# Kernel optimization log

Measured on AMD Instinct MI355X. Metric: run time of the kernel, lower is better.

## Reference

```python
import jax, jax.numpy as jnp
import numpy as np

B, S, D, H = 2, 2048, 1024, 16
DK = D // H

def setup_inputs() -> dict:
    key = jax.random.key(0)
    ks = jax.random.split(key, 11)
    s = 1.0 / np.sqrt(D)
    inp = {
        'q': jax.random.normal(ks[0], (B, S, D), jnp.float32),
        'k': jax.random.normal(ks[1], (B, S, D), jnp.float32),
        'v': jax.random.normal(ks[2], (B, S, D), jnp.float32),
        'mask': jnp.tril(jnp.ones((S, S), jnp.bool_))[None, None],  # [1,1,S,S] causal
        'w_q': jax.random.normal(ks[3], (D, D), jnp.float32) * s,
        'b_q': jax.random.normal(ks[4], (D,), jnp.float32) * s,
        'w_k': jax.random.normal(ks[5], (D, D), jnp.float32) * s,
        'b_k': jax.random.normal(ks[6], (D,), jnp.float32) * s,
        'w_v': jax.random.normal(ks[7], (D, D), jnp.float32) * s,
        'b_v': jax.random.normal(ks[8], (D,), jnp.float32) * s,
        'w_o': jax.random.normal(ks[9], (D, D), jnp.float32) * s,
        'b_o': jax.random.normal(ks[10], (D,), jnp.float32) * s,
    }
    return inp

def reference(q, k, v, mask, w_q, b_q, w_k, b_k, w_v, b_v, w_o, b_o):
    # Linear projections (torch Linear: x @ W^T + b)
    qh = (q @ w_q.T + b_q).reshape(B, S, H, DK).transpose(0, 2, 1, 3)  # [B,H,S,DK]
    kh = (k @ w_k.T + b_k).reshape(B, S, H, DK).transpose(0, 2, 1, 3)
    vh = (v @ w_v.T + b_v).reshape(B, S, H, DK).transpose(0, 2, 1, 3)
    scores = jnp.einsum('bhqd,bhkd->bhqk', qh, kh) / jnp.sqrt(jnp.float32(DK))
    scores = jnp.where(mask, scores, jnp.float32(-jnp.inf))
    attn = jax.nn.softmax(scores, axis=-1)  # dropout p=0.0 -> identity
    out = jnp.einsum('bhqk,bhkd->bhqd', attn, vh)
    out = out.transpose(0, 2, 1, 3).reshape(B, S, D)
    return out @ w_o.T + b_o
```

## Files before the change

### kernel.cpp

```cpp
#include <hip/hip_runtime.h>
#include <hip/hip_bf16.h>

typedef __bf16 bf16_t;
typedef __bf16 bf16x4 __attribute__((ext_vector_type(4)));
typedef __bf16 bf16x8 __attribute__((ext_vector_type(8)));
typedef float f32x4 __attribute__((ext_vector_type(4)));

#define B_ 2
#define S_ 2048
#define D_ 1024
#define H_ 16
#define DK_ 64
#define M_ (B_ * S_)

__device__ __forceinline__ f32x4 mfma16(bf16x8 a, bf16x8 b, f32x4 c) {
  return __builtin_amdgcn_mfma_f32_16x16x32_bf16(a, b, c, 0, 0, 0);
}

__device__ __forceinline__ void async_load16(const bf16_t* g, bf16_t* l) {
  __builtin_amdgcn_global_load_lds(
      (const __attribute__((address_space(1))) void*)g,
      (__attribute__((address_space(3))) void*)l, 16, 0, 0);
}


__global__ void cvt_all(const float* __restrict__ q, const float* __restrict__ k,
                        const float* __restrict__ v, const float* __restrict__ w0,
                        const float* __restrict__ w1, const float* __restrict__ w2,
                        const float* __restrict__ w3, bf16_t* __restrict__ qb,
                        bf16_t* __restrict__ kb, bf16_t* __restrict__ vb,
                        bf16_t* __restrict__ o0, bf16_t* __restrict__ o1,
                        bf16_t* __restrict__ o2, bf16_t* __restrict__ o3) {
  const int y = blockIdx.y;
  if (y >= 3 && blockIdx.x >= 512) return;
  const float* src;
  bf16_t* dst;
  float sc = 1.0f;
  switch (y) {
    case 0: src = q; dst = qb; break;
    case 1: src = k; dst = kb; break;
    case 2: src = v; dst = vb; break;
    case 3: src = w0; dst = o0; sc = 0.125f; break;
    case 4: src = w1; dst = o1; break;
    case 5: src = w2; dst = o2; break;
    default: src = w3; dst = o3; break;
  }
  long i = ((long)blockIdx.x * blockDim.x + threadIdx.x) * 8;
  const float4* s4 = (const float4*)(src + i);
  float4 a = s4[0], b = s4[1];
  bf16x8 o;
  o[0] = (bf16_t)(a.x * sc); o[1] = (bf16_t)(a.y * sc);
  o[2] = (bf16_t)(a.z * sc); o[3] = (bf16_t)(a.w * sc);
  o[4] = (bf16_t)(b.x * sc); o[5] = (bf16_t)(b.y * sc);
  o[6] = (bf16_t)(b.z * sc); o[7] = (bf16_t)(b.w * sc);
  *(bf16x8*)(dst + i) = o;
}


__device__ __forceinline__ int swzG(int b) {
  return b ^ (((b >> 7) & 7) << 4);
}

template <int NR>
__device__ __forceinline__ void stage_tile(const bf16_t* g, bf16_t* lds,
                                           const int* srcoff, int wave) {
#pragma unroll
  for (int rnd = 0; rnd < NR; ++rnd)
    async_load16(g + srcoff[rnd], lds + rnd * 2048 + wave * 512);
}

template <int MODE>
__device__ __forceinline__ void gemm_core(const bf16_t* __restrict__ A,
                                          const bf16_t* __restrict__ W,
                                          const float* __restrict__ bias,
                                          float bscale, void* __restrict__ Cv,
                                          bf16_t* __restrict__ As,
                                          bf16_t* __restrict__ Bs) {
  constexpr int N = 1024, K = 1024;
  constexpr int TILE = 128 * 32;
  constexpr int NIT = K / 32;
  const int tid = threadIdx.x;
  const int wave = tid >> 6, lane = tid & 63;
  const int quad = lane >> 4, l15 = lane & 15;
  const int wm = wave >> 1, wn = wave & 1;
  const int bm = blockIdx.x * 128, bn = blockIdx.y * 128;

  f32x4 acc[4][4] = {};

  int srcoff[2];
#pragma unroll
  for (int rnd = 0; rnd < 2; ++rnd) {
    const int bb = rnd * 4096 + tid * 16;
    const int sb = swzG(bb);
    srcoff[rnd] = (sb >> 6) * K + ((sb & 63) >> 1);
  }
  const bf16_t* ag = A + (long)bm * K;
  const bf16_t* bg = W + (long)bn * K;

  const int xorv = ((l15 >> 1) & 7) << 4;
  const int aco = (((wm * 64 + l15) * 64 + quad * 16) ^ xorv) >> 1;
  const int bco = (((wn * 64 + l15) * 64 + quad * 16) ^ xorv) >> 1;

  stage_tile<2>(ag, As, srcoff, wave);
  stage_tile<2>(bg, Bs, srcoff, wave);
  stage_tile<2>(ag + 32, As + TILE, srcoff, wave);
  stage_tile<2>(bg + 32, Bs + TILE, srcoff, wave);

  int rb = 0, sb2 = 2;
  for (int j = 0; j < NIT; ++j) {
    if (j < NIT - 1)
      asm volatile("s_waitcnt vmcnt(4)" ::: "memory");
    else
      asm volatile("s_waitcnt vmcnt(0)" ::: "memory");
    __builtin_amdgcn_sched_barrier(0);
    __builtin_amdgcn_s_barrier();
    __builtin_amdgcn_sched_barrier(0);

    if (j + 2 < NIT) {
      const int kk2 = (j + 2) * 32;
      stage_tile<2>(ag + kk2, As + sb2 * TILE, srcoff, wave);
      stage_tile<2>(bg + kk2, Bs + sb2 * TILE, srcoff, wave);
    }
    sb2 = (sb2 == 2) ? 0 : sb2 + 1;

    const bf16_t* Ac = As + rb * TILE;
    const bf16_t* Bc = Bs + rb * TILE;
    rb = (rb == 2) ? 0 : rb + 1;
    bf16x8 af[4], bfr[4];
#pragma unroll
    for (int i = 0; i < 4; ++i)
      af[i] = *(const bf16x8*)&Ac[aco + i * 512];
#pragma unroll
    for (int i = 0; i < 4; ++i)
      bfr[i] = *(const bf16x8*)&Bc[bco + i * 512];
    __builtin_amdgcn_s_setprio(1);
#pragma unroll
    for (int mi = 0; mi < 4; ++mi)
#pragma unroll
      for (int ni = 0; ni < 4; ++ni)
        acc[mi][ni] = mfma16(af[mi], bfr[ni], acc[mi][ni]);
    __builtin_amdgcn_s_setprio(0);
  }

#pragma unroll
  for (int mi = 0; mi < 4; ++mi) {
#pragma unroll
    for (int ni = 0; ni < 4; ++ni) {
      const int col = bn + wn * 64 + ni * 16 + l15;
      const float bsv = bias[col] * bscale;
      f32x4 v = acc[mi][ni];
      const int row0 = bm + wm * 64 + mi * 16 + quad * 4;
      if (MODE == 3) {
        float* C = (float*)Cv;
#pragma unroll
        for (int r = 0; r < 4; ++r)
          C[(long)(row0 + r) * N + col] = v[r] + bsv;
      } else if (MODE == 1) {
        bf16_t* C = (bf16_t*)Cv;
        const int hh = col >> 6, dk = col & 63;
        const int bq = row0 >> 11, s0 = row0 & 2047;
        bf16_t* base = C + (((long)bq * H_ + hh) * S_ + s0) * DK_ + dk;
#pragma unroll
        for (int r = 0; r < 4; ++r)
          base[(long)r * DK_] = (bf16_t)(v[r] + bsv);
      } else {
        bf16_t* C = (bf16_t*)Cv;
        const int hh = col >> 6, dk = col & 63;
        const int bq = row0 >> 11, s0 = row0 & 2047;
        bf16x4 pk;
#pragma unroll
        for (int r = 0; r < 4; ++r) pk[r] = (bf16_t)(v[r] + bsv);
        *(bf16x4*)(C + (((long)bq * H_ + hh) * DK_ + dk) * S_ + s0) = pk;
      }
    }
  }
}

__global__ __launch_bounds__(256) void gemm_qkv(
    const bf16_t* __restrict__ qb, const bf16_t* __restrict__ kb,
    const bf16_t* __restrict__ vb, const bf16_t* __restrict__ wq,
    const bf16_t* __restrict__ wk, const bf16_t* __restrict__ wv,
    const float* __restrict__ biq, const float* __restrict__ bik,
    const float* __restrict__ biv, bf16_t* __restrict__ Qh,
    bf16_t* __restrict__ Kh, bf16_t* __restrict__ Vt) {
  __shared__ bf16_t As[3][128 * 32];
  __shared__ bf16_t Bs[3][128 * 32];
  if (blockIdx.z == 0)
    gemm_core<1>(qb, wq, biq, 0.125f, Qh, &As[0][0], &Bs[0][0]);
  else if (blockIdx.z == 1)
    gemm_core<1>(kb, wk, bik, 1.0f, Kh, &As[0][0], &Bs[0][0]);
  else
    gemm_core<2>(vb, wv, biv, 1.0f, Vt, &As[0][0], &Bs[0][0]);
}

__device__ __forceinline__ int swzG128(int b) {
  return b ^ (((b >> 7) & 7) << 4);
}

__global__ __launch_bounds__(256) void gemm_out64(
    const bf16_t* __restrict__ AO, const bf16_t* __restrict__ wo,
    const float* __restrict__ bo, float* __restrict__ out) {
  constexpr int N = 1024, K = 1024;
  constexpr int ATILE = 64 * 64, BTILE = 128 * 64;
  constexpr int NIT = K / 64;
  __shared__ bf16_t As[3][ATILE];
  __shared__ bf16_t Bs[3][BTILE];
  const int tid = threadIdx.x;
  const int wave = tid >> 6, lane = tid & 63;
  const int quad = lane >> 4, l15 = lane & 15;
  const int wm = wave >> 1, wn = wave & 1;
  const int bm = blockIdx.x * 64, bn = blockIdx.y * 128;

  f32x4 acc[2][4] = {};

  int srcoff[4];
#pragma unroll
  for (int rnd = 0; rnd < 4; ++rnd) {
    const int bb = rnd * 4096 + tid * 16;
    const int sb = swzG128(bb);
    srcoff[rnd] = (sb >> 7) * K + ((sb & 127) >> 1);
  }
  const bf16_t* ag = AO + (long)bm * K;
  const bf16_t* bg = wo + (long)bn * K;

  const int co0 = ((quad * 16) ^ ((l15 & 7) << 4)) >> 1;
  const int co1 = ((quad * 16 + 64) ^ ((l15 & 7) << 4)) >> 1;
  const int arow0 = (wm * 32 + l15) * 64;
  const int brow0 = (wn * 64 + l15) * 64;

  stage_tile<2>(ag, &As[0][0], srcoff, wave);
  stage_tile<4>(bg, &Bs[0][0], srcoff, wave);
  stage_tile<2>(ag + 64, &As[1][0], srcoff, wave);
  stage_tile<4>(bg + 64, &Bs[1][0], srcoff, wave);

  int rb = 0, sb2 = 2;
  for (int j = 0; j < NIT; ++j) {
    if (j < NIT - 1)
      asm volatile("s_waitcnt vmcnt(6)" ::: "memory");
    else
      asm volatile("s_waitcnt vmcnt(0)" ::: "memory");
    __builtin_amdgcn_sched_barrier(0);
    __builtin_amdgcn_s_barrier();
    __builtin_amdgcn_sched_barrier(0);

    if (j + 2 < NIT) {
      const int kk2 = (j + 2) * 64;
      stage_tile<2>(ag + kk2, &As[sb2][0], srcoff, wave);
      stage_tile<4>(bg + kk2, &Bs[sb2][0], srcoff, wave);
    }
    sb2 = (sb2 == 2) ? 0 : sb2 + 1;

    const bf16_t* Ac = &As[rb][0];
    const bf16_t* Bc = &Bs[rb][0];
    rb = (rb == 2) ? 0 : rb + 1;
#pragma unroll
    for (int h = 0; h < 2; ++h) {
      const int co = h ? co1 : co0;
      bf16x8 af[2], bfr[4];
#pragma unroll
      for (int i = 0; i < 2; ++i)
        af[i] = *(const bf16x8*)&Ac[arow0 + i * 1024 + co];
#pragma unroll
      for (int i = 0; i < 4; ++i)
        bfr[i] = *(const bf16x8*)&Bc[brow0 + i * 1024 + co];
      __builtin_amdgcn_s_setprio(1);
#pragma unroll
      for (int mi = 0; mi < 2; ++mi)
#pragma unroll
        for (int ni = 0; ni < 4; ++ni)
          acc[mi][ni] = mfma16(af[mi], bfr[ni], acc[mi][ni]);
      __builtin_amdgcn_s_setprio(0);
    }
  }

#pragma unroll
  for (int mi = 0; mi < 2; ++mi) {
#pragma unroll
    for (int ni = 0; ni < 4; ++ni) {
      const int col = bn + wn * 64 + ni * 16 + l15;
      const float bsv = bo[col];
      f32x4 v = acc[mi][ni];
      const int row0 = bm + wm * 32 + mi * 16 + quad * 4;
#pragma unroll
      for (int r = 0; r < 4; ++r)
        out[(long)(row0 + r) * N + col] = v[r] + bsv;
    }
  }
}


__device__ __forceinline__ int swzK(int b) {
  return b ^ (((b >> 7) & 3) << 4) ^ (((b >> 10) & 1) << 6);
}
__device__ __forceinline__ int swzV(int b) {
  return b ^ (((b >> 7) & 7) << 4);
}

template <bool MASKED>
__device__ __forceinline__ void softmax_pa(const f32x4 st[4], float& l_i,
                                           bf16x8& pa0, bf16x8& pa1,
                                           const int qcol, const int quad) {
#pragma unroll
  for (int nb = 0; nb < 4; ++nb) {
    const int kvb = quad * 8 + (nb & 1) * 4 + (nb >> 1) * 32;
#pragma unroll
    for (int r = 0; r < 4; ++r) {
      float x = st[nb][r];
      if (MASKED && (kvb + r) > qcol) x = -30000.f;
      const float pv = __expf(x);
      l_i += pv;
      const bf16_t pb = (bf16_t)pv;
      const int idx = ((nb & 1) << 2) | r;
      if (nb < 2) pa0[idx] = pb;
      else        pa1[idx] = pb;
    }
  }
}

__global__ __launch_bounds__(256, 3) void flash_attn3(
    const bf16_t* __restrict__ Qh, const bf16_t* __restrict__ Kh,
    const bf16_t* __restrict__ Vt, bf16_t* __restrict__ Po,
    float* __restrict__ Pl) {
  const int bid = blockIdx.x;
  const int g = bid & 31;
  const int z = bid >> 5;
  const int i = z / 3, pi = z % 3;
  const int h = g & 15, b = g >> 4;
  const int tA = i, tB = 31 - i;
  const int tid = threadIdx.x, wave = tid >> 6, lane = tid & 63;
  const int quad = lane >> 4, l15 = lane & 15;
  const int qcol = wave * 16 + l15;
  const int prow = ((l15 >> 2) << 3) | (l15 & 3);

  __shared__ bf16_t Kls[2][64 * 64];
  __shared__ bf16_t Vls[2][64 * 64];

  const bf16_t* qhead = Qh + ((long)(b * H_ + h) * S_) * DK_;
  const bf16_t* khead = Kh + ((long)(b * H_ + h) * S_) * DK_;
  const bf16_t* vhead = Vt + ((long)(b * H_ + h) * DK_) * S_;

  int koffe[2], voffe[2], ldse[2];
#pragma unroll
  for (int c = 0; c < 2; ++c) {
    const int bb = c * 4096 + wave * 1024 + lane * 16;
    koffe[c] = swzK(bb) >> 1;
    const int vs = swzV(bb);
    voffe[c] = (vs >> 7) * S_ + ((vs & 127) >> 1);
    ldse[c] = c * 2048 + wave * 512;
  }

  int kro[4][2], vro[4][2];
#pragma unroll
  for (int nb = 0; nb < 4; ++nb) {
    const int krow = prow + (nb & 1) * 4 + (nb >> 1) * 32;
    const int vrow = nb * 16 + l15;
#pragma unroll
    for (int hh = 0; hh < 2; ++hh) {
      kro[nb][hh] = swzK(krow * 128 + quad * 16 + hh * 64) >> 1;
      vro[nb][hh] = swzV(vrow * 128 + quad * 16 + hh * 64) >> 1;
    }
  }

  const int qA = tA * 64 + wave * 16;
  const int qB = tB * 64 + wave * 16;
  const bf16_t* qpA = qhead + (long)(qA + l15) * DK_ + quad * 8;
  const bf16_t* qpB = qhead + (long)(qB + l15) * DK_ + quad * 8;
  const bf16x8 aqA0 = *(const bf16x8*)qpA;
  const bf16x8 aqA1 = *(const bf16x8*)(qpA + 32);
  const bf16x8 aqB0 = *(const bf16x8*)qpB;
  const bf16x8 aqB1 = *(const bf16x8*)(qpB + 32);

  f32x4 oA[4] = {}, oB[4] = {};
  float lA = 0.f, lB = 0.f;

  {
    const bf16_t* kt = khead + pi * (64 * DK_);
    const bf16_t* vt = vhead + pi * 64;
#pragma unroll
    for (int c = 0; c < 2; ++c) {
      async_load16(kt + koffe[c], &Kls[0][ldse[c]]);
      async_load16(vt + voffe[c], &Vls[0][ldse[c]]);
    }
  }

  int cur = 0;
  for (int j = pi; j <= tB; j += 3) {
    const bool pf = (j + 3 <= tB);
    if (pf) {
      const bf16_t* kt = khead + (j + 3) * (64 * DK_);
      const bf16_t* vt = vhead + (j + 3) * 64;
#pragma unroll
      for (int c = 0; c < 2; ++c) {
        async_load16(kt + koffe[c], &Kls[cur ^ 1][ldse[c]]);
        async_load16(vt + voffe[c], &Vls[cur ^ 1][ldse[c]]);
      }
      asm volatile("s_waitcnt vmcnt(4)" ::: "memory");
    } else {
      asm volatile("s_waitcnt vmcnt(0)" ::: "memory");
    }
    __builtin_amdgcn_sched_barrier(0);
    __builtin_amdgcn_s_barrier();
    __builtin_amdgcn_sched_barrier(0);

    const bf16_t* Kc = &Kls[cur][0];
    const bf16_t* Vc = &Vls[cur][0];

    bf16x8 k0[4], k1[4];
#pragma unroll
    for (int nb = 0; nb < 4; ++nb) {
      k0[nb] = *(const bf16x8*)&Kc[kro[nb][0]];
      k1[nb] = *(const bf16x8*)&Kc[kro[nb][1]];
    }

    bf16x8 paB0, paB1, paA0, paA1;
    {
      f32x4 stB[4];
#pragma unroll
      for (int nb = 0; nb < 4; ++nb) {
        f32x4 t = {};
        t = mfma16(k0[nb], aqB0, t);
        t = mfma16(k1[nb], aqB1, t);
        stB[nb] = t;
      }
      if (j == tB)
        softmax_pa<true>(stB, lB, paB0, paB1, qcol, quad);
      else
        softmax_pa<false>(stB, lB, paB0, paB1, qcol, quad);
    }
    const bool doA = (j <= tA);
    if (doA) {
      f32x4 stA[4];
#pragma unroll
      for (int nb = 0; nb < 4; ++nb) {
        f32x4 t = {};
        t = mfma16(k0[nb], aqA0, t);
        t = mfma16(k1[nb], aqA1, t);
        stA[nb] = t;
      }
      if (j == tA)
        softmax_pa<true>(stA, lA, paA0, paA1, qcol, quad);
      else
        softmax_pa<false>(stA, lA, paA0, paA1, qcol, quad);
    }

    bf16x8 v0[4], v1[4];
#pragma unroll
    for (int nb = 0; nb < 4; ++nb) {
      v0[nb] = *(const bf16x8*)&Vc[vro[nb][0]];
      v1[nb] = *(const bf16x8*)&Vc[vro[nb][1]];
    }
#pragma unroll
    for (int nb = 0; nb < 4; ++nb) {
      oB[nb] = mfma16(paB0, v0[nb], oB[nb]);
      oB[nb] = mfma16(paB1, v1[nb], oB[nb]);
    }
    if (doA) {
#pragma unroll
      for (int nb = 0; nb < 4; ++nb) {
        oA[nb] = mfma16(paA0, v0[nb], oA[nb]);
        oA[nb] = mfma16(paA1, v1[nb], oA[nb]);
      }
    }

    asm volatile("s_waitcnt lgkmcnt(0)" ::: "memory");
    __builtin_amdgcn_sched_barrier(0);
    __builtin_amdgcn_s_barrier();
    __builtin_amdgcn_sched_barrier(0);
    cur ^= 1;
  }

  lA += __shfl_xor(lA, 16, 64);
  lA += __shfl_xor(lA, 32, 64);
  lB += __shfl_xor(lB, 16, 64);
  lB += __shfl_xor(lB, 32, 64);

  bf16_t* po = Po + (long)pi * (M_ * D_);
  bf16_t* poA = po + (long)(b * S_ + qA + quad * 4) * D_ + h * DK_ + l15;
  bf16_t* poB = po + (long)(b * S_ + qB + quad * 4) * D_ + h * DK_ + l15;
#pragma unroll
  for (int r = 0; r < 4; ++r) {
#pragma unroll
    for (int nb = 0; nb < 4; ++nb) {
      poA[(long)r * D_ + nb * 16] = (bf16_t)oA[nb][r];
      poB[(long)r * D_ + nb * 16] = (bf16_t)oB[nb][r];
    }
  }

  if (quad == 0) {
    float* pl = Pl + (long)pi * (B_ * H_ * S_) + (long)(b * H_ + h) * S_;
    pl[qA + l15] = lA;
    pl[qB + l15] = lB;
  }
}


__global__ __launch_bounds__(256) void merge_po(const bf16_t* __restrict__ Po,
                                                const float* __restrict__ Pl,
                                                bf16_t* __restrict__ AO) {
  const long e = ((long)blockIdx.x * 256 + threadIdx.x) * 8;
  const int bs = (int)(e >> 10);
  const int d = (int)(e & 1023);
  const int h = d >> 6;
  const int b = bs >> 11, s = bs & 2047;
  const long lidx = ((long)(b * H_ + h)) * S_ + s;

  float acc[8] = {0.f, 0.f, 0.f, 0.f, 0.f, 0.f, 0.f, 0.f};
  float L = 0.f;
#pragma unroll
  for (int p = 0; p < 3; ++p) {
    bf16x8 x = *(const bf16x8*)(Po + (long)p * (M_ * D_) + e);
#pragma unroll
    for (int k = 0; k < 8; ++k) acc[k] += (float)x[k];
    L += Pl[(long)p * (B_ * H_ * S_) + lidx];
  }
  const float inv = 1.f / L;
  bf16x8 y;
#pragma unroll
  for (int k = 0; k < 8; ++k) y[k] = (bf16_t)(acc[k] * inv);
  *(bf16x8*)(AO + e) = y;
}


extern "C" void kernel_launch(void* const* d_in, const int* in_sizes, int n_in,
                              void* d_out, int out_size, void* d_ws, size_t ws_size,
                              hipStream_t stream) {
  const float* q = (const float*)d_in[0];
  const float* k = (const float*)d_in[1];
  const float* v = (const float*)d_in[2];
  const float* wq = (const float*)d_in[4];
  const float* bq = (const float*)d_in[5];
  const float* wk = (const float*)d_in[6];
  const float* bk = (const float*)d_in[7];
  const float* wv = (const float*)d_in[8];
  const float* bv = (const float*)d_in[9];
  const float* wo = (const float*)d_in[10];
  const float* bo = (const float*)d_in[11];
  float* out = (float*)d_out;

  char* ws = (char*)d_ws;
  const size_t MB = 1024 * 1024;
  bf16_t* Qh = (bf16_t*)(ws);
  bf16_t* Kh = (bf16_t*)(ws + 8 * MB);
  bf16_t* Vt = (bf16_t*)(ws + 16 * MB);
  bf16_t* AO = (bf16_t*)(ws + 24 * MB);
  bf16_t* qb = (bf16_t*)(ws + 32 * MB);
  bf16_t* kb = (bf16_t*)(ws + 40 * MB);
  bf16_t* vb = (bf16_t*)(ws + 48 * MB);
  bf16_t* wqb = (bf16_t*)(ws + 56 * MB);
  bf16_t* wkb = (bf16_t*)(ws + 58 * MB);
  bf16_t* wvb = (bf16_t*)(ws + 60 * MB);
  bf16_t* wob = (bf16_t*)(ws + 62 * MB);
  bf16_t* Po = (bf16_t*)(ws + 32 * MB);
  float* Pl = (float*)(ws + 56 * MB);

  cvt_all<<<dim3(2048, 7, 1), 256, 0, stream>>>(q, k, v, wq, wk, wv, wo, qb, kb,
                                                vb, wqb, wkb, wvb, wob);
  gemm_qkv<<<dim3(32, 8, 3), 256, 0, stream>>>(qb, kb, vb, wqb, wkb, wvb, bq, bk,
                                               bv, Qh, Kh, Vt);
  flash_attn3<<<dim3(1536, 1, 1), 256, 0, stream>>>(Qh, Kh, Vt, Po, Pl);
  merge_po<<<dim3(2048, 1, 1), 256, 0, stream>>>(Po, Pl, AO);
  gemm_out64<<<dim3(64, 8, 1), 256, 0, stream>>>(AO, wob, bo, out);
}
```

Before: 216.9 us.

## Fuse partial-output merge into output GEMM and triple-buffer flash attention K/V

Removes the merge_po kernel. The output-projection GEMM now loads the three bf16 partial outputs and their row sums directly, normalizes them in registers and writes the A tile into LDS, so the AO intermediate never round-trips through global memory. The cost is that each of the 8 N-blocks re-reads and re-merges the same A rows (three times the A-side traffic plus the Pl loads), and register pressure rises. Separately, flash attention moves from two to three K/V LDS buffers with a prefetch distance of two tiles, which drops the trailing barrier per iteration. This uses more LDS per block, which may affect the occupancy of 3 blocks per CU.

```diff
diff --git a/kernel.cpp b/kernel.cpp
--- a/kernel.cpp
+++ b/kernel.cpp
@@ -193,15 +193,18 @@
     gemm_core<2>(vb, wv, biv, 1.0f, Vt, &As[0][0], &Bs[0][0]);
 }
 
+
 __device__ __forceinline__ int swzG128(int b) {
   return b ^ (((b >> 7) & 7) << 4);
 }
 
 __global__ __launch_bounds__(256) void gemm_out64(
-    const bf16_t* __restrict__ AO, const bf16_t* __restrict__ wo,
-    const float* __restrict__ bo, float* __restrict__ out) {
+    const bf16_t* __restrict__ Po, const float* __restrict__ Pl,
+    const bf16_t* __restrict__ wo, const float* __restrict__ bo,
+    float* __restrict__ out) {
   constexpr int N = 1024, K = 1024;
-  constexpr int ATILE = 64 * 64, BTILE = 128 * 64;
+  constexpr int ATILE = 64 * 64;
+  constexpr int BTILE = 128 * 64;
   constexpr int NIT = K / 64;
   __shared__ bf16_t As[3][ATILE];
   __shared__ bf16_t Bs[3][BTILE];
@@ -220,39 +223,74 @@
     const int sb = swzG128(bb);
     srcoff[rnd] = (sb >> 7) * K + ((sb & 127) >> 1);
   }
-  const bf16_t* ag = AO + (long)bm * K;
   const bf16_t* bg = wo + (long)bn * K;
+
+  const int arow_[2] = {(tid * 16) >> 7, (4096 + tid * 16) >> 7};
+  const int acol_[2] = {((tid * 16) & 127) >> 1, ((4096 + tid * 16) & 127) >> 1};
+  const int awr_[2] = {swzG128(tid * 16) >> 1, swzG128(4096 + tid * 16) >> 1};
 
   const int co0 = ((quad * 16) ^ ((l15 & 7) << 4)) >> 1;
   const int co1 = ((quad * 16 + 64) ^ ((l15 & 7) << 4)) >> 1;
   const int arow0 = (wm * 32 + l15) * 64;
   const int brow0 = (wn * 64 + l15) * 64;
 
-  stage_tile<2>(ag, &As[0][0], srcoff, wave);
+  bf16x8 apo[2][3];
+  float apl[2][3];
+
+  auto issueA = [&](int t) {
+#pragma unroll
+    for (int c = 0; c < 2; ++c) {
+      const int m = bm + arow_[c];
+      const long e = (long)m * D_ + t * 64 + acol_[c];
+      const long pidx = (long)((m >> 11) * H_ + t) * S_ + (m & 2047);
+#pragma unroll
+      for (int p = 0; p < 3; ++p) {
+        apo[c][p] = *(const bf16x8*)(Po + (long)p * (M_ * D_) + e);
+        apl[c][p] = Pl[(long)p * (B_ * H_ * S_) + pidx];
+      }
+    }
+  };
+  auto mathWriteA = [&](bf16_t* dst) {
+#pragma unroll
+    for (int c = 0; c < 2; ++c) {
+      const float L = apl[c][0] + apl[c][1] + apl[c][2];
+      const float inv = 1.0f / L;
+      bf16x8 y;
+#pragma unroll
+      for (int kx = 0; kx < 8; ++kx) {
+        const float s = (float)apo[c][0][kx] + (float)apo[c][1][kx] +
+                        (float)apo[c][2][kx];
+        y[kx] = (bf16_t)(s * inv);
+      }
+      *(bf16x8*)(dst + awr_[c]) = y;
+    }
+  };
+
+  issueA(0);
   stage_tile<4>(bg, &Bs[0][0], srcoff, wave);
-  stage_tile<2>(ag + 64, &As[1][0], srcoff, wave);
+  mathWriteA(&As[0][0]);
+  issueA(1);
   stage_tile<4>(bg + 64, &Bs[1][0], srcoff, wave);
 
-  int rb = 0, sb2 = 2;
   for (int j = 0; j < NIT; ++j) {
+    if (j + 1 < NIT) mathWriteA(&As[(j + 1) % 3][0]);
     if (j < NIT - 1)
-      asm volatile("s_waitcnt vmcnt(6)" ::: "memory");
+      asm volatile("s_waitcnt vmcnt(4)" ::: "memory");
     else
       asm volatile("s_waitcnt vmcnt(0)" ::: "memory");
+    asm volatile("s_waitcnt lgkmcnt(0)" ::: "memory");
     __builtin_amdgcn_sched_barrier(0);
     __builtin_amdgcn_s_barrier();
     __builtin_amdgcn_sched_barrier(0);
 
     if (j + 2 < NIT) {
-      const int kk2 = (j + 2) * 64;
-      stage_tile<2>(ag + kk2, &As[sb2][0], srcoff, wave);
-      stage_tile<4>(bg + kk2, &Bs[sb2][0], srcoff, wave);
-    }
-    sb2 = (sb2 == 2) ? 0 : sb2 + 1;
-
-    const bf16_t* Ac = &As[rb][0];
-    const bf16_t* Bc = &Bs[rb][0];
-    rb = (rb == 2) ? 0 : rb + 1;
+      issueA(j + 2);
+      stage_tile<4>(bg + (j + 2) * 64, &Bs[(j + 2) % 3][0], srcoff, wave);
+    }
+    __builtin_amdgcn_sched_barrier(0);
+
+    const bf16_t* Ac = &As[j % 3][0];
+    const bf16_t* Bc = &Bs[j % 3][0];
 #pragma unroll
     for (int h = 0; h < 2; ++h) {
       const int co = h ? co1 : co0;
@@ -332,8 +370,8 @@
   const int qcol = wave * 16 + l15;
   const int prow = ((l15 >> 2) << 3) | (l15 & 3);
 
-  __shared__ bf16_t Kls[2][64 * 64];
-  __shared__ bf16_t Vls[2][64 * 64];
+  __shared__ bf16_t Kls[3][64 * 64];
+  __shared__ bf16_t Vls[3][64 * 64];
 
   const bf16_t* qhead = Qh + ((long)(b * H_ + h) * S_) * DK_;
   const bf16_t* khead = Kh + ((long)(b * H_ + h) * S_) * DK_;
@@ -373,37 +411,42 @@
   f32x4 oA[4] = {}, oB[4] = {};
   float lA = 0.f, lB = 0.f;
 
-  {
-    const bf16_t* kt = khead + pi * (64 * DK_);
-    const bf16_t* vt = vhead + pi * 64;
-#pragma unroll
-    for (int c = 0; c < 2; ++c) {
-      async_load16(kt + koffe[c], &Kls[0][ldse[c]]);
-      async_load16(vt + voffe[c], &Vls[0][ldse[c]]);
-    }
-  }
-
-  int cur = 0;
+#pragma unroll
+  for (int c = 0; c < 2; ++c) {
+    async_load16(khead + pi * (64 * DK_) + koffe[c], &Kls[0][ldse[c]]);
+    async_load16(vhead + pi * 64 + voffe[c], &Vls[0][ldse[c]]);
+  }
+#pragma unroll
+  for (int c = 0; c < 2; ++c) {
+    async_load16(khead + (pi + 3) * (64 * DK_) + koffe[c], &Kls[1][ldse[c]]);
+    async_load16(vhead + (pi + 3) * 64 + voffe[c], &Vls[1][ldse[c]]);
+  }
+
+  int bi = 0;
   for (int j = pi; j <= tB; j += 3) {
     const bool pf = (j + 3 <= tB);
-    if (pf) {
-      const bf16_t* kt = khead + (j + 3) * (64 * DK_);
-      const bf16_t* vt = vhead + (j + 3) * 64;
+    if (pf)
+      asm volatile("s_waitcnt vmcnt(4)" ::: "memory");
+    else
+      asm volatile("s_waitcnt vmcnt(0)" ::: "memory");
+    __builtin_amdgcn_sched_barrier(0);
+    __builtin_amdgcn_s_barrier();
+    __builtin_amdgcn_sched_barrier(0);
+
+    if (j + 6 <= tB) {
+      const int tb2 = (bi == 0) ? 2 : (bi - 1);
+      const bf16_t* kt = khead + (j + 6) * (64 * DK_);
+      const bf16_t* vt = vhead + (j + 6) * 64;
 #pragma unroll
       for (int c = 0; c < 2; ++c) {
-        async_load16(kt + koffe[c], &Kls[cur ^ 1][ldse[c]]);
-        async_load16(vt + voffe[c], &Vls[cur ^ 1][ldse[c]]);
-      }
-      asm volatile("s_waitcnt vmcnt(4)" ::: "memory");
-    } else {
-      asm volatile("s_waitcnt vmcnt(0)" ::: "memory");
-    }
-    __builtin_amdgcn_sched_barrier(0);
-    __builtin_amdgcn_s_barrier();
-    __builtin_amdgcn_sched_barrier(0);
-
-    const bf16_t* Kc = &Kls[cur][0];
-    const bf16_t* Vc = &Vls[cur][0];
+        async_load16(kt + koffe[c], &Kls[tb2][ldse[c]]);
+        async_load16(vt + voffe[c], &Vls[tb2][ldse[c]]);
+      }
+    }
+    __builtin_amdgcn_sched_barrier(0);
+
+    const bf16_t* Kc = &Kls[bi][0];
+    const bf16_t* Vc = &Vls[bi][0];
 
     bf16x8 k0[4], k1[4];
 #pragma unroll
@@ -462,11 +505,7 @@
       }
     }
 
-    asm volatile("s_waitcnt lgkmcnt(0)" ::: "memory");
-    __builtin_amdgcn_sched_barrier(0);
-    __builtin_amdgcn_s_barrier();
-    __builtin_amdgcn_sched_barrier(0);
-    cur ^= 1;
+    bi = (bi == 2) ? 0 : bi + 1;
   }
 
   lA += __shfl_xor(lA, 16, 64);
@@ -491,33 +530,6 @@
     pl[qA + l15] = lA;
     pl[qB + l15] = lB;
   }
-}
-
-
-__global__ __launch_bounds__(256) void merge_po(const bf16_t* __restrict__ Po,
-                                                const float* __restrict__ Pl,
-                                                bf16_t* __restrict__ AO) {
-  const long e = ((long)blockIdx.x * 256 + threadIdx.x) * 8;
-  const int bs = (int)(e >> 10);
-  const int d = (int)(e & 1023);
-  const int h = d >> 6;
-  const int b = bs >> 11, s = bs & 2047;
-  const long lidx = ((long)(b * H_ + h)) * S_ + s;
-
-  float acc[8] = {0.f, 0.f, 0.f, 0.f, 0.f, 0.f, 0.f, 0.f};
-  float L = 0.f;
-#pragma unroll
-  for (int p = 0; p < 3; ++p) {
-    bf16x8 x = *(const bf16x8*)(Po + (long)p * (M_ * D_) + e);
-#pragma unroll
-    for (int k = 0; k < 8; ++k) acc[k] += (float)x[k];
-    L += Pl[(long)p * (B_ * H_ * S_) + lidx];
-  }
-  const float inv = 1.f / L;
-  bf16x8 y;
-#pragma unroll
-  for (int k = 0; k < 8; ++k) y[k] = (bf16_t)(acc[k] * inv);
-  *(bf16x8*)(AO + e) = y;
 }
 
 
@@ -542,7 +554,6 @@
   bf16_t* Qh = (bf16_t*)(ws);
   bf16_t* Kh = (bf16_t*)(ws + 8 * MB);
   bf16_t* Vt = (bf16_t*)(ws + 16 * MB);
-  bf16_t* AO = (bf16_t*)(ws + 24 * MB);
   bf16_t* qb = (bf16_t*)(ws + 32 * MB);
   bf16_t* kb = (bf16_t*)(ws + 40 * MB);
   bf16_t* vb = (bf16_t*)(ws + 48 * MB);
@@ -558,6 +569,5 @@
   gemm_qkv<<<dim3(32, 8, 3), 256, 0, stream>>>(qb, kb, vb, wqb, wkb, wvb, bq, bk,
                                                bv, Qh, Kh, Vt);
   flash_attn3<<<dim3(1536, 1, 1), 256, 0, stream>>>(Qh, Kh, Vt, Po, Pl);
-  merge_po<<<dim3(2048, 1, 1), 256, 0, stream>>>(Po, Pl, AO);
-  gemm_out64<<<dim3(64, 8, 1), 256, 0, stream>>>(AO, wob, bo, out);
-}
+  gemm_out64<<<dim3(64, 8, 1), 256, 0, stream>>>(Po, Pl, wob, bo, out);
+}
```

Result: no change. 213.7 us (-1.5%).

## Drop KV split in flash attention, fuse normalization, triple-buffer K/V

Applied to the files above, without the earlier changes.

Removes the three-way KV-split of the attention kernel and the separate merge kernel. Each block now walks all KV tiles for its paired query tiles and normalizes output in registers before writing AO directly. The K/V LDS ring grows from two to three buffers, with one barrier per iteration and prefetch two tiles ahead. This cuts the partial-output write/read traffic and a kernel launch, at the cost of fewer blocks (512 vs 1536), lower occupancy hint, and longer serial loops per block.

```diff
diff --git a/kernel.cpp b/kernel.cpp
--- a/kernel.cpp
+++ b/kernel.cpp
@@ -193,6 +193,7 @@
     gemm_core<2>(vb, wv, biv, 1.0f, Vt, &As[0][0], &Bs[0][0]);
 }
 
+
 __device__ __forceinline__ int swzG128(int b) {
   return b ^ (((b >> 7) & 7) << 4);
 }
@@ -317,14 +318,12 @@
   }
 }
 
-__global__ __launch_bounds__(256, 3) void flash_attn3(
+__global__ __launch_bounds__(256, 2) void flash_attn3(
     const bf16_t* __restrict__ Qh, const bf16_t* __restrict__ Kh,
-    const bf16_t* __restrict__ Vt, bf16_t* __restrict__ Po,
-    float* __restrict__ Pl) {
+    const bf16_t* __restrict__ Vt, bf16_t* __restrict__ AO) {
   const int bid = blockIdx.x;
   const int g = bid & 31;
-  const int z = bid >> 5;
-  const int i = z / 3, pi = z % 3;
+  const int i = bid >> 5;
   const int h = g & 15, b = g >> 4;
   const int tA = i, tB = 31 - i;
   const int tid = threadIdx.x, wave = tid >> 6, lane = tid & 63;
@@ -332,8 +331,8 @@
   const int qcol = wave * 16 + l15;
   const int prow = ((l15 >> 2) << 3) | (l15 & 3);
 
-  __shared__ bf16_t Kls[2][64 * 64];
-  __shared__ bf16_t Vls[2][64 * 64];
+  __shared__ bf16_t Kls[3][64 * 64];
+  __shared__ bf16_t Vls[3][64 * 64];
 
   const bf16_t* qhead = Qh + ((long)(b * H_ + h) * S_) * DK_;
   const bf16_t* khead = Kh + ((long)(b * H_ + h) * S_) * DK_;
@@ -373,37 +372,41 @@
   f32x4 oA[4] = {}, oB[4] = {};
   float lA = 0.f, lB = 0.f;
 
-  {
-    const bf16_t* kt = khead + pi * (64 * DK_);
-    const bf16_t* vt = vhead + pi * 64;
-#pragma unroll
-    for (int c = 0; c < 2; ++c) {
-      async_load16(kt + koffe[c], &Kls[0][ldse[c]]);
-      async_load16(vt + voffe[c], &Vls[0][ldse[c]]);
-    }
-  }
-
-  int cur = 0;
-  for (int j = pi; j <= tB; j += 3) {
-    const bool pf = (j + 3 <= tB);
-    if (pf) {
-      const bf16_t* kt = khead + (j + 3) * (64 * DK_);
-      const bf16_t* vt = vhead + (j + 3) * 64;
+#pragma unroll
+  for (int c = 0; c < 2; ++c) {
+    async_load16(khead + koffe[c], &Kls[0][ldse[c]]);
+    async_load16(vhead + voffe[c], &Vls[0][ldse[c]]);
+  }
+#pragma unroll
+  for (int c = 0; c < 2; ++c) {
+    async_load16(khead + 64 * DK_ + koffe[c], &Kls[1][ldse[c]]);
+    async_load16(vhead + 64 + voffe[c], &Vls[1][ldse[c]]);
+  }
+
+  int bi = 0;
+  for (int j = 0; j <= tB; ++j) {
+    if (j < tB)
+      asm volatile("s_waitcnt vmcnt(4)" ::: "memory");
+    else
+      asm volatile("s_waitcnt vmcnt(0)" ::: "memory");
+    __builtin_amdgcn_sched_barrier(0);
+    __builtin_amdgcn_s_barrier();
+    __builtin_amdgcn_sched_barrier(0);
+
+    if (j + 2 <= tB) {
+      const int tb2 = (bi == 0) ? 2 : (bi - 1);
+      const bf16_t* kt = khead + (j + 2) * (64 * DK_);
+      const bf16_t* vt = vhead + (j + 2) * 64;
 #pragma unroll
       for (int c = 0; c < 2; ++c) {
-        async_load16(kt + koffe[c], &Kls[cur ^ 1][ldse[c]]);
-        async_load16(vt + voffe[c], &Vls[cur ^ 1][ldse[c]]);
+        async_load16(kt + koffe[c], &Kls[tb2][ldse[c]]);
+        async_load16(vt + voffe[c], &Vls[tb2][ldse[c]]);
       }
-      asm volatile("s_waitcnt vmcnt(4)" ::: "memory");
-    } else {
-      asm volatile("s_waitcnt vmcnt(0)" ::: "memory");
-    }
-    __builtin_amdgcn_sched_barrier(0);
-    __builtin_amdgcn_s_barrier();
-    __builtin_amdgcn_sched_barrier(0);
-
-    const bf16_t* Kc = &Kls[cur][0];
-    const bf16_t* Vc = &Vls[cur][0];
+    }
+    __builtin_amdgcn_sched_barrier(0);
+
+    const bf16_t* Kc = &Kls[bi][0];
+    const bf16_t* Vc = &Vls[bi][0];
 
     bf16x8 k0[4], k1[4];
 #pragma unroll
@@ -462,11 +465,7 @@
       }
     }
 
-    asm volatile("s_waitcnt lgkmcnt(0)" ::: "memory");
-    __builtin_amdgcn_sched_barrier(0);
-    __builtin_amdgcn_s_barrier();
-    __builtin_amdgcn_sched_barrier(0);
-    cur ^= 1;
+    bi = (bi == 2) ? 0 : bi + 1;
   }
 
   lA += __shfl_xor(lA, 16, 64);
@@ -474,50 +473,18 @@
   lB += __shfl_xor(lB, 16, 64);
   lB += __shfl_xor(lB, 32, 64);
 
-  bf16_t* po = Po + (long)pi * (M_ * D_);
-  bf16_t* poA = po + (long)(b * S_ + qA + quad * 4) * D_ + h * DK_ + l15;
-  bf16_t* poB = po + (long)(b * S_ + qB + quad * 4) * D_ + h * DK_ + l15;
+  bf16_t* aoA = AO + (long)(b * S_ + qA + quad * 4) * D_ + h * DK_ + l15;
+  bf16_t* aoB = AO + (long)(b * S_ + qB + quad * 4) * D_ + h * DK_ + l15;
 #pragma unroll
   for (int r = 0; r < 4; ++r) {
+    const float invA = 1.0f / __shfl(lA, quad * 4 + r, 64);
+    const float invB = 1.0f / __shfl(lB, quad * 4 + r, 64);
 #pragma unroll
     for (int nb = 0; nb < 4; ++nb) {
-      poA[(long)r * D_ + nb * 16] = (bf16_t)oA[nb][r];
-      poB[(long)r * D_ + nb * 16] = (bf16_t)oB[nb][r];
-    }
-  }
-
-  if (quad == 0) {
-    float* pl = Pl + (long)pi * (B_ * H_ * S_) + (long)(b * H_ + h) * S_;
-    pl[qA + l15] = lA;
-    pl[qB + l15] = lB;
-  }
-}
-
-
-__global__ __launch_bounds__(256) void merge_po(const bf16_t* __restrict__ Po,
-                                                const float* __restrict__ Pl,
-                                                bf16_t* __restrict__ AO) {
-  const long e = ((long)blockIdx.x * 256 + threadIdx.x) * 8;
-  const int bs = (int)(e >> 10);
-  const int d = (int)(e & 1023);
-  const int h = d >> 6;
-  const int b = bs >> 11, s = bs & 2047;
-  const long lidx = ((long)(b * H_ + h)) * S_ + s;
-
-  float acc[8] = {0.f, 0.f, 0.f, 0.f, 0.f, 0.f, 0.f, 0.f};
-  float L = 0.f;
-#pragma unroll
-  for (int p = 0; p < 3; ++p) {
-    bf16x8 x = *(const bf16x8*)(Po + (long)p * (M_ * D_) + e);
-#pragma unroll
-    for (int k = 0; k < 8; ++k) acc[k] += (float)x[k];
-    L += Pl[(long)p * (B_ * H_ * S_) + lidx];
-  }
-  const float inv = 1.f / L;
-  bf16x8 y;
-#pragma unroll
-  for (int k = 0; k < 8; ++k) y[k] = (bf16_t)(acc[k] * inv);
-  *(bf16x8*)(AO + e) = y;
+      aoA[(long)r * D_ + nb * 16] = (bf16_t)(oA[nb][r] * invA);
+      aoB[(long)r * D_ + nb * 16] = (bf16_t)(oB[nb][r] * invB);
+    }
+  }
 }
 
 
@@ -550,14 +517,11 @@
   bf16_t* wkb = (bf16_t*)(ws + 58 * MB);
   bf16_t* wvb = (bf16_t*)(ws + 60 * MB);
   bf16_t* wob = (bf16_t*)(ws + 62 * MB);
-  bf16_t* Po = (bf16_t*)(ws + 32 * MB);
-  float* Pl = (float*)(ws + 56 * MB);
 
   cvt_all<<<dim3(2048, 7, 1), 256, 0, stream>>>(q, k, v, wq, wk, wv, wo, qb, kb,
                                                 vb, wqb, wkb, wvb, wob);
   gemm_qkv<<<dim3(32, 8, 3), 256, 0, stream>>>(qb, kb, vb, wqb, wkb, wvb, bq, bk,
                                                bv, Qh, Kh, Vt);
-  flash_attn3<<<dim3(1536, 1, 1), 256, 0, stream>>>(Qh, Kh, Vt, Po, Pl);
-  merge_po<<<dim3(2048, 1, 1), 256, 0, stream>>>(Po, Pl, AO);
+  flash_attn3<<<dim3(512, 1, 1), 256, 0, stream>>>(Qh, Kh, Vt, AO);
   gemm_out64<<<dim3(64, 8, 1), 256, 0, stream>>>(AO, wob, bo, out);
 }
```

Result: faster. 210.3 us (-3.1%).
